# Performance work log

Measured on AMD Instinct MI355X. Metric: run time of the kernel, lower is better.

The kernel has to match this reference:

```python
import jax, jax.numpy as jnp
import numpy as np
import math

N = 10000      # atoms
E = 320000     # neighbor pairs (edges)
NELEM = 3      # species one-hot size
NRAD = 8       # radial channels per component
NB = 8         # bessel basis size
ZETA = 4       # max angular moment
RC = 5.0       # radial cutoff
S = 4          # species embedding size (species_layer_sizes[-1])
NCOMP = (ZETA + 2) * NRAD   # 2-body slice + (ZETA+1) angular slices = 48
FEAT = NCOMP * S            # 192

# multinomial expansion of (r_i . r_j)^l : lxlylz powers and l!/(lx!ly!lz!) norms
_TERMS = []
for l in range(ZETA + 1):
    pw, nm = [], []
    for a in range(l + 1):
        for b in range(l + 1 - a):
            c = l - a - b
            pw.append((a, b, c))
            nm.append(math.factorial(l) / (math.factorial(a) * math.factorial(b) * math.factorial(c)))
    _TERMS.append((np.array(pw, dtype=np.float32), np.array(nm, dtype=np.float32)))


def _silu(x):
    return x * jax.nn.sigmoid(x)


def setup_inputs() -> dict:
    key = jax.random.key(0)
    ks = jax.random.split(key, 12)
    rij = (jax.random.uniform(ks[0], (E, 3), minval=-1.0, maxval=1.0) * (RC / math.sqrt(3.0))).astype(jnp.float32)
    first_atom = jax.random.randint(ks[1], (E,), 0, N, dtype=jnp.int32)
    second_atom = jax.random.randint(ks[2], (E,), 0, N, dtype=jnp.int32)
    species_idx = jax.random.randint(ks[3], (N,), 0, NELEM, dtype=jnp.int32)
    w = lambda k, s: (jax.random.normal(k, s) * 0.1).astype(jnp.float32)
    z = lambda s: jnp.zeros(s, jnp.float32)
    return dict(
        rij=rij, species_idx=species_idx, first_atom=first_atom, second_atom=second_atom,
        Wr1=w(ks[4], (NB, 64)), br1=z((64,)),
        Wr2=w(ks[5], (64, NCOMP)), br2=z((NCOMP,)),
        Ws1=w(ks[6], (NELEM, 16)), bs1=z((16,)),
        Ws2=w(ks[7], (16, S)), bs2=z((S,)),
        Wa1=w(ks[8], (FEAT, 64)), ba1=z((64,)),
        Wa2=w(ks[9], (64, 64)), ba2=z((64,)),
        Wa3=w(ks[10], (64, 1)), ba3=z((1,)),
    )


def reference(rij, species_idx, first_atom, second_atom,
              Wr1, br1, Wr2, br2, Ws1, bs1, Ws2, bs2,
              Wa1, ba1, Wa2, ba2, Wa3, ba3):
    d = jnp.sqrt(jnp.sum(rij * rij, axis=-1) + 1e-12)            # [E]
    rhat = rij / d[:, None]                                       # [E,3]
    fc = jnp.where(d < RC, 0.5 * (jnp.cos(np.pi * d / RC) + 1.0), 0.0)
    n = jnp.arange(1, NB + 1, dtype=rij.dtype)
    bes = jnp.sqrt(2.0 / RC) * jnp.sin(n[None, :] * np.pi * d[:, None] / RC) / d[:, None]  # [E,NB]
    # learned radial functions, all components at once, smoothed by cutoff
    R = _silu(_silu(bes @ Wr1 + br1) @ Wr2 + br2) * fc[:, None]   # [E, NCOMP]
    # species encoder -> per-atom embedding, gathered on neighbor atom j
    onehot = jax.nn.one_hot(species_idx, NELEM, dtype=rij.dtype)  # [N,NELEM]
    semb = jnp.tanh(onehot @ Ws1 + bs1) @ Ws2 + bs2               # [N,S]
    sj = semb[second_atom]                                        # [E,S]
    # 2-body feature
    feats = [jax.ops.segment_sum(R[:, :NRAD, None] * sj[:, None, :], first_atom, num_segments=N)]  # [N,NRAD,S]
    off = NRAD
    for l in range(ZETA + 1):
        pw, nm = _TERMS[l]
        comps = jnp.prod(rhat[:, None, :] ** jnp.asarray(pw)[None, :, :], axis=-1)  # [E,C_l]
        Rl = R[:, off:off + NRAD]
        off += NRAD
        edge = Rl[:, :, None, None] * comps[:, None, :, None] * sj[:, None, None, :]  # [E,NRAD,C_l,S]
        A = jax.ops.segment_sum(edge, first_atom, num_segments=N)                     # [N,NRAD,C_l,S]
        feats.append(jnp.einsum('nrcs,c->nrs', A * A, jnp.asarray(nm)))               # [N,NRAD,S]
    feat = jnp.concatenate(feats, axis=1).reshape(N, -1)          # [N, FEAT]
    h = _silu(feat @ Wa1 + ba1)
    h = _silu(h @ Wa2 + ba2)
    return (h @ Wa3 + ba3)[:, 0]                                  # per-atom energies [N]
```

## Files before the change

kernel.cpp:

```cpp
#include <hip/hip_runtime.h>
#include <math.h>

#define NATOMS 10000
#define NEDGES 320000
#define NBINS  (NATOMS * 4)
#define RC_F 5.0f
#define PI_F 3.14159265358979323846f

#define WS_SEMB   0
#define WS_GTOT   12
#define WS_CNT    16
#define WS_OFFS   40016
#define WS_CURSOR 80016
#define WS_EIDX   120016
#define WS_SA     440096
#define WS_SB     10680096

__device__ __constant__ int   d_PWA[35] = {0, 0,0,1, 0,0,0,1,1,2, 0,0,0,0,1,1,1,2,2,3, 0,0,0,0,0,1,1,1,1,2,2,2,3,3,4};
__device__ __constant__ int   d_PWB[35] = {0, 0,1,0, 0,1,2,0,1,0, 0,1,2,3,0,1,2,0,1,0, 0,1,2,3,4,0,1,2,3,0,1,2,0,1,0};
__device__ __constant__ int   d_PWC[35] = {0, 1,0,0, 2,1,0,1,0,0, 3,2,1,0,2,1,0,1,0,0, 4,3,2,1,0,3,2,1,0,2,1,0,1,0,0};
__device__ __constant__ float d_NM[35]  = {1.f, 1.f,1.f,1.f, 1.f,2.f,1.f,2.f,2.f,1.f,
                                           1.f,3.f,3.f,1.f,3.f,6.f,3.f,3.f,3.f,1.f,
                                           1.f,4.f,6.f,4.f,1.f,4.f,12.f,12.f,4.f,6.f,12.f,6.f,4.f,4.f,1.f};
__device__ __constant__ int   d_LBLK[35]= {0, 1,1,1, 2,2,2,2,2,2, 3,3,3,3,3,3,3,3,3,3, 4,4,4,4,4,4,4,4,4,4,4,4,4,4,4};
__device__ __constant__ int   d_L6[6]   = {0,1,4,10,20,35};

__device__ __forceinline__ float siluf(float x) { return x / (1.0f + __expf(-x)); }

__device__ __forceinline__ float2 f2fma(float2 a, float2 b, float2 c) {
  return make_float2(fmaf(a.x, b.x, c.x), fmaf(a.y, b.y, c.y));
}

__device__ __forceinline__ float psel(float x, int p) {
  float x2 = x * x;
  float r = 1.0f;
  r = (p == 1) ? x : r;
  r = (p == 2) ? x2 : r;
  r = (p == 3) ? x2 * x : r;
  r = (p == 4) ? x2 * x2 : r;
  return r;
}

__global__ void k_init(const float* __restrict__ Ws1, const float* __restrict__ bs1,
                       const float* __restrict__ Ws2, const float* __restrict__ bs2,
                       float* __restrict__ ws)
{
  int tid = blockIdx.x * blockDim.x + threadIdx.x;
  int* cnt = (int*)(ws + WS_CNT);
  if (tid < NBINS) cnt[tid] = 0;
  if (tid == 0) *(int*)(ws + WS_GTOT) = 0;
  if (tid < 12) {
    int t = tid >> 2, s = tid & 3;
    float acc = bs2[s];
    for (int j = 0; j < 16; j++) acc += tanhf(Ws1[t * 16 + j] + bs1[j]) * Ws2[j * 4 + s];
    ws[WS_SEMB + tid] = acc;
  }
}

__global__ void k_hist(const int* __restrict__ first_atom, const int* __restrict__ second_atom,
                       const int* __restrict__ species, float* __restrict__ ws)
{
  int e = blockIdx.x * blockDim.x + threadIdx.x;
  if (e < NEDGES) {
    int* cnt = (int*)(ws + WS_CNT);
    int bin = first_atom[e] * 4 + species[second_atom[e]];
    atomicAdd(&cnt[bin], 1);
  }
}

__global__ __launch_bounds__(256) void k_alloc(float* __restrict__ ws)
{
  const int4* cnt4 = (const int4*)(ws + WS_CNT);
  int4* offs4   = (int4*)(ws + WS_OFFS);
  int4* cursor4 = (int4*)(ws + WS_CURSOR);
  int* gtot = (int*)(ws + WS_GTOT);
  __shared__ int wsum[4];
  __shared__ int sbase;
  int tid = threadIdx.x;
  int lane = tid & 63, wv = tid >> 6;
  int a = blockIdx.x * 256 + tid;
  bool live = (a < NATOMS);
  int4 c = live ? cnt4[a] : make_int4(0, 0, 0, 0);
  int s = c.x + c.y + c.z + c.w;
  int inc = s;
  #pragma unroll
  for (int d = 1; d < 64; d <<= 1) {
    int v = __shfl_up(inc, d, 64);
    if (lane >= d) inc += v;
  }
  if (lane == 63) wsum[wv] = inc;
  __syncthreads();
  if (tid == 0) sbase = atomicAdd(gtot, wsum[0] + wsum[1] + wsum[2] + wsum[3]);
  __syncthreads();
  int woff = sbase;
  for (int w = 0; w < wv; w++) woff += wsum[w];
  int o0 = woff + inc - s;
  if (live) {
    int4 o;
    o.x = o0;
    o.y = o.x + c.x;
    o.z = o.y + c.y;
    o.w = o.z + c.z;
    offs4[a] = o;
    cursor4[a] = o;
  }
}

__global__ __launch_bounds__(256) void k_edge(
    const float* __restrict__ rij, const int* __restrict__ species,
    const int* __restrict__ first_atom, const int* __restrict__ second_atom,
    const float* __restrict__ Wr1, const float* __restrict__ br1,
    const float* __restrict__ Wr2, const float* __restrict__ br2,
    float* __restrict__ ws)
{
  __shared__ __align__(16) float sRec[4][64 * 28];
  int tid = threadIdx.x, lane = tid & 63, wv = tid >> 6;
  int e = blockIdx.x * 256 + tid;
  int* cursor = (int*)(ws + WS_CURSOR);
  int* eidx   = (int*)(ws + WS_EIDX);
  float* myrow = &sRec[wv][lane * 28];

  int a = first_atom[e];
  int t = species[second_atom[e]];
  int pos = atomicAdd(&cursor[a * 4 + t], 1);
  eidx[pos] = e;

  float x = rij[e * 3 + 0], y = rij[e * 3 + 1], z = rij[e * 3 + 2];
  float d = sqrtf(x * x + y * y + z * z + 1e-12f);
  float invd = 1.0f / d;

  float theta = (PI_F / RC_F) * d;
  float s1 = __sinf(theta), c1 = __cosf(theta);
  float fc = (d < RC_F) ? 0.5f * (c1 + 1.0f) : 0.0f;
  float bes[8];
  {
    float sq = sqrtf(2.0f / RC_F) * invd;
    float twoc = 2.0f * c1;
    float sp = 0.0f, sc = s1;
    #pragma unroll
    for (int k = 0; k < 8; k++) {
      bes[k] = sq * sc;
      float sn = twoc * sc - sp;
      sp = sc; sc = sn;
    }
  }

  float h1[64];
  #pragma unroll
  for (int j4 = 0; j4 < 16; j4++) {
    float2 a01 = *(const float2*)&br1[j4 * 4];
    float2 a23 = *(const float2*)&br1[j4 * 4 + 2];
    #pragma unroll
    for (int k = 0; k < 8; k++) {
      float2 b2 = make_float2(bes[k], bes[k]);
      a01 = f2fma(b2, *(const float2*)&Wr1[k * 64 + j4 * 4],     a01);
      a23 = f2fma(b2, *(const float2*)&Wr1[k * 64 + j4 * 4 + 2], a23);
    }
    h1[j4 * 4 + 0] = siluf(a01.x);
    h1[j4 * 4 + 1] = siluf(a01.y);
    h1[j4 * 4 + 2] = siluf(a23.x);
    h1[j4 * 4 + 3] = siluf(a23.y);
  }

  int ebase = blockIdx.x * 256 + wv * 64;
  const float* buf = &sRec[wv][0];
  int f4 = lane & 7;

  for (int j4 = 0; j4 < 6; j4++) {
    float2 a01 = *(const float2*)&br2[j4 * 4];
    float2 a23 = *(const float2*)&br2[j4 * 4 + 2];
    #pragma unroll
    for (int k = 0; k < 64; k++) {
      float2 h2 = make_float2(h1[k], h1[k]);
      a01 = f2fma(h2, *(const float2*)&Wr2[k * 48 + j4 * 4],     a01);
      a23 = f2fma(h2, *(const float2*)&Wr2[k * 48 + j4 * 4 + 2], a23);
    }
    *(float4*)(myrow + j4 * 4) = make_float4(siluf(a01.x) * fc, siluf(a01.y) * fc,
                                             siluf(a23.x) * fc, siluf(a23.y) * fc);
  }
  {
    float* gbase = ws + WS_SA + (size_t)ebase * 32;
    if (f4 < 6) {
      #pragma unroll
      for (int q = 0; q < 8; q++) {
        int g4 = q * 64 + lane;
        float4 v = *(const float4*)(buf + (g4 >> 3) * 28 + f4 * 4);
        *(float4*)(gbase + (size_t)g4 * 4) = v;
      }
    }
  }

  for (int j4 = 6; j4 < 12; j4++) {
    float2 a01 = *(const float2*)&br2[j4 * 4];
    float2 a23 = *(const float2*)&br2[j4 * 4 + 2];
    #pragma unroll
    for (int k = 0; k < 64; k++) {
      float2 h2 = make_float2(h1[k], h1[k]);
      a01 = f2fma(h2, *(const float2*)&Wr2[k * 48 + j4 * 4],     a01);
      a23 = f2fma(h2, *(const float2*)&Wr2[k * 48 + j4 * 4 + 2], a23);
    }
    *(float4*)(myrow + (j4 - 6) * 4) = make_float4(siluf(a01.x) * fc, siluf(a01.y) * fc,
                                                   siluf(a23.x) * fc, siluf(a23.y) * fc);
  }
  *(float4*)(myrow + 24) = make_float4(x * invd, y * invd, z * invd, 0.0f);
  {
    float* gbase = ws + WS_SB + (size_t)ebase * 32;
    if (f4 < 7) {
      #pragma unroll
      for (int q = 0; q < 8; q++) {
        int g4 = q * 64 + lane;
        float4 v = *(const float4*)(buf + (g4 >> 3) * 28 + f4 * 4);
        *(float4*)(gbase + (size_t)g4 * 4) = v;
      }
    }
  }
}

__global__ __launch_bounds__(128) void k_atom(
    const float* __restrict__ ws,
    const float* __restrict__ Wa1, const float* __restrict__ ba1,
    const float* __restrict__ Wa2, const float* __restrict__ ba2,
    const float* __restrict__ Wa3, const float* __restrict__ ba3,
    float* __restrict__ out)
{
  __shared__ __align__(16) float sScr[2][1920];
  int tid = threadIdx.x;
  int lane = tid & 63, wv = tid >> 6;
  int a = blockIdx.x * 2 + wv;
  float* sStage = &sScr[wv][0];
  float* sG     = &sScr[wv][768];
  float* sFeat  = &sScr[wv][1632];
  float* sH     = &sScr[wv][1824];

  const int* eidx = (const int*)(ws + WS_EIDX);
  int4 o = ((const int4*)(ws + WS_OFFS))[a];

  const int c = lane;
  bool isc = (c < 35);
  int pa = 0, pb = 0, pcw = 0, lb = 0;
  if (isc) { pa = d_PWA[c]; pb = d_PWB[c]; pcw = d_PWC[c]; lb = d_LBLK[c]; }
  int rdir = lane - 35;
  bool isd = (rdir >= 0) && (rdir < 8);
  int rl = lane >> 4, fl = lane & 15;
  const float* gsrc = ws + (fl < 6 ? WS_SA : WS_SB);
  int foff = (fl < 6) ? fl : ((fl < 13) ? fl - 6 : 6);

  float2 g2[3][4];
  #pragma unroll
  for (int t2 = 0; t2 < 3; t2++)
    #pragma unroll
    for (int r = 0; r < 4; r++) g2[t2][r] = make_float2(0.f, 0.f);
  float g0[3] = {0.0f, 0.0f, 0.0f};

#define CORE(T) {                                                             \
    const float* rb = buf + j * 64;                                           \
    if (isc) {                                                                \
      float comp = psel(rb[48], pa) * psel(rb[49], pb) * psel(rb[50], pcw);   \
      float2 c2 = make_float2(comp, comp);                                    \
      const float2* r2 = (const float2*)(rb + 8 + 8 * lb);                    \
      g2[T][0] = f2fma(c2, r2[0], g2[T][0]);                                  \
      g2[T][1] = f2fma(c2, r2[1], g2[T][1]);                                  \
      g2[T][2] = f2fma(c2, r2[2], g2[T][2]);                                  \
      g2[T][3] = f2fma(c2, r2[3], g2[T][3]);                                  \
    } else if (isd) {                                                         \
      g0[T] += rb[rdir];                                                      \
    }                                                                         \
  }

#define LOADR(Q, DST) {                                                       \
    int sl_ = (Q) * 4 + rl; if (sl_ >= m) sl_ = m - 1;                        \
    int pk_ = __shfl(packed, sl_, 64);                                        \
    DST = *(const float4*)(gsrc + (size_t)pk_ * 32 + foff * 4);               \
  }

#define RUN(T, LO, HI)                                                        \
  for (int cb = (LO); cb < (HI); cb += 64) {                                  \
    int m = (HI) - cb; if (m > 64) m = 64;                                    \
    int pp = cb + lane;                                                       \
    int packed = eidx[pp < (HI) ? pp : (LO)];                                 \
    int R = (m + 3) >> 2;                                                     \
    float4 v0, v1;                                                            \
    LOADR(0, v0)                                                              \
    if (R > 1) { LOADR(1, v1) } else v1 = v0;                                 \
    int bsel = 0;                                                             \
    for (int r = 0; r < R; r++) {                                             \
      float* buf = sStage + (bsel << 8);                                      \
      bsel = (bsel == 2) ? 0 : bsel + 1;                                      \
      *(float4*)(buf + rl * 64 + fl * 4) = v0;                                \
      v0 = v1;                                                                \
      if (r + 2 < R) LOADR(r + 2, v1)                                         \
      int g = r * 4, gm = m - g; if (gm > 4) gm = 4;                          \
      for (int j = 0; j < gm; j++) CORE(T)                                    \
    }                                                                         \
  }

  RUN(0, o.x, o.y)
  RUN(1, o.y, o.z)
  RUN(2, o.z, o.w)
#undef RUN
#undef CORE
#undef LOADR

  if (isc) {
    #pragma unroll
    for (int t2 = 0; t2 < 3; t2++)
      #pragma unroll
      for (int r = 0; r < 8; r++) {
        float gval = (r & 1) ? g2[t2][r >> 1].y : g2[t2][r >> 1].x;
        sG[(t2 * 8 + r) * 36 + c] = gval;
      }
  } else if (isd) {
    #pragma unroll
    for (int t2 = 0; t2 < 3; t2++) sG[(t2 * 8 + rdir) * 36 + 35] = g0[t2];
  }

  int s = lane & 3;
  float se0 = ws[WS_SEMB + s], se1 = ws[WS_SEMB + 4 + s], se2 = ws[WS_SEMB + 8 + s];
  float fout[3];
  #pragma unroll
  for (int u = 0; u < 3; u++) {
    int f = lane + 64 * u;
    int blk = f >> 5, rr = (f >> 2) & 7;
    float acc;
    if (blk == 0) {
      acc = se0 * sG[(0 + rr) * 36 + 35] + se1 * sG[(8 + rr) * 36 + 35] + se2 * sG[(16 + rr) * 36 + 35];
    } else {
      int c0 = d_L6[blk - 1], c1 = d_L6[blk];
      acc = 0.0f;
      for (int cc = c0; cc < c1; cc++) {
        float A = se0 * sG[(0 + rr) * 36 + cc] + se1 * sG[(8 + rr) * 36 + cc] + se2 * sG[(16 + rr) * 36 + cc];
        acc += d_NM[cc] * A * A;
      }
    }
    fout[u] = acc;
  }
  #pragma unroll
  for (int u = 0; u < 3; u++) sFeat[lane + 64 * u] = fout[u];

  {
    float a0 = 0.f, a1 = 0.f, a2 = 0.f, a3 = 0.f;
    for (int k4 = 0; k4 < 48; k4++) {
      float4 f4 = *(const float4*)(sFeat + k4 * 4);
      const float* w = Wa1 + (k4 * 4) * 64 + lane;
      a0 += f4.x * w[0];
      a1 += f4.y * w[64];
      a2 += f4.z * w[128];
      a3 += f4.w * w[192];
    }
    sH[lane] = siluf(a0 + a1 + a2 + a3 + ba1[lane]);
  }

  {
    float a0 = 0.f, a1 = 0.f, a2 = 0.f, a3 = 0.f;
    for (int k4 = 0; k4 < 16; k4++) {
      float4 h4 = *(const float4*)(sH + k4 * 4);
      const float* w = Wa2 + (k4 * 4) * 64 + lane;
      a0 += h4.x * w[0];
      a1 += h4.y * w[64];
      a2 += h4.z * w[128];
      a3 += h4.w * w[192];
    }
    float h2 = siluf(a0 + a1 + a2 + a3 + ba2[lane]);
    float pr = h2 * Wa3[lane];
    #pragma unroll
    for (int off = 32; off > 0; off >>= 1) pr += __shfl_down(pr, off, 64);
    if (lane == 0) out[a] = pr + ba3[0];
  }
}

extern "C" void kernel_launch(void* const* d_in, const int* in_sizes, int n_in,
                              void* d_out, int out_size, void* d_ws, size_t ws_size,
                              hipStream_t stream)
{
  const float* rij         = (const float*)d_in[0];
  const int*   species     = (const int*)  d_in[1];
  const int*   first_atom  = (const int*)  d_in[2];
  const int*   second_atom = (const int*)  d_in[3];
  const float* Wr1 = (const float*)d_in[4];
  const float* br1 = (const float*)d_in[5];
  const float* Wr2 = (const float*)d_in[6];
  const float* br2 = (const float*)d_in[7];
  const float* Ws1 = (const float*)d_in[8];
  const float* bs1 = (const float*)d_in[9];
  const float* Ws2 = (const float*)d_in[10];
  const float* bs2 = (const float*)d_in[11];
  const float* Wa1 = (const float*)d_in[12];
  const float* ba1 = (const float*)d_in[13];
  const float* Wa2 = (const float*)d_in[14];
  const float* ba2 = (const float*)d_in[15];
  const float* Wa3 = (const float*)d_in[16];
  const float* ba3 = (const float*)d_in[17];
  float* ws  = (float*)d_ws;
  float* out = (float*)d_out;

  k_init<<<(NBINS + 255) / 256, 256, 0, stream>>>(Ws1, bs1, Ws2, bs2, ws);
  k_hist<<<(NEDGES + 255) / 256, 256, 0, stream>>>(first_atom, second_atom, species, ws);
  k_alloc<<<(NATOMS + 255) / 256, 256, 0, stream>>>(ws);
  k_edge<<<NEDGES / 256, 256, 0, stream>>>(rij, species, first_atom, second_atom,
                                           Wr1, br1, Wr2, br2, ws);
  k_atom<<<NATOMS / 2, 128, 0, stream>>>(ws, Wa1, ba1, Wa2, ba2, Wa3, ba3, out);
}
```

Measured before the change: 213.7 us.

## Process four atoms per block and share MLP weight loads across waves

```diff
diff --git a/kernel.cpp b/kernel.cpp
--- a/kernel.cpp
+++ b/kernel.cpp
@@ -216,21 +216,25 @@
   }
 }
 
-__global__ __launch_bounds__(128) void k_atom(
+__global__ __launch_bounds__(256) void k_atom(
     const float* __restrict__ ws,
     const float* __restrict__ Wa1, const float* __restrict__ ba1,
     const float* __restrict__ Wa2, const float* __restrict__ ba2,
     const float* __restrict__ Wa3, const float* __restrict__ ba3,
     float* __restrict__ out)
 {
-  __shared__ __align__(16) float sScr[2][1920];
+  __shared__ __align__(16) float sStage[4][768];
+  __shared__ __align__(16) float sG[4][864];
+  __shared__ __align__(16) float sFeat[4][192];
+  __shared__ __align__(16) float sP[4][4][64];
+  __shared__ __align__(16) float sH[4][64];
+  __shared__ float sSemb[12];
   int tid = threadIdx.x;
   int lane = tid & 63, wv = tid >> 6;
-  int a = blockIdx.x * 2 + wv;
-  float* sStage = &sScr[wv][0];
-  float* sG     = &sScr[wv][768];
-  float* sFeat  = &sScr[wv][1632];
-  float* sH     = &sScr[wv][1824];
+  int a = blockIdx.x * 4 + wv;
+  float* sStg = sStage[wv];
+  float* sGw  = sG[wv];
+  if (tid < 12) sSemb[tid] = ws[WS_SEMB + tid];
 
   const int* eidx = (const int*)(ws + WS_EIDX);
   int4 o = ((const int4*)(ws + WS_OFFS))[a];
@@ -284,7 +288,7 @@
     if (R > 1) { LOADR(1, v1) } else v1 = v0;                                 \
     int bsel = 0;                                                             \
     for (int r = 0; r < R; r++) {                                             \
-      float* buf = sStage + (bsel << 8);                                      \
+      float* buf = sStg + (bsel << 8);                                        \
       bsel = (bsel == 2) ? 0 : bsel + 1;                                      \
       *(float4*)(buf + rl * 64 + fl * 4) = v0;                                \
       v0 = v1;                                                                \
@@ -307,61 +311,95 @@
       #pragma unroll
       for (int r = 0; r < 8; r++) {
         float gval = (r & 1) ? g2[t2][r >> 1].y : g2[t2][r >> 1].x;
-        sG[(t2 * 8 + r) * 36 + c] = gval;
+        sGw[(t2 * 8 + r) * 36 + c] = gval;
       }
   } else if (isd) {
     #pragma unroll
-    for (int t2 = 0; t2 < 3; t2++) sG[(t2 * 8 + rdir) * 36 + 35] = g0[t2];
-  }
-
-  int s = lane & 3;
-  float se0 = ws[WS_SEMB + s], se1 = ws[WS_SEMB + 4 + s], se2 = ws[WS_SEMB + 8 + s];
-  float fout[3];
+    for (int t2 = 0; t2 < 3; t2++) sGw[(t2 * 8 + rdir) * 36 + 35] = g0[t2];
+  }
+  __syncthreads();
+
   #pragma unroll
   for (int u = 0; u < 3; u++) {
-    int f = lane + 64 * u;
-    int blk = f >> 5, rr = (f >> 2) & 7;
+    int idx = tid + 256 * u;
+    int i = idx / 192;
+    int f = idx - i * 192;
+    int s = f & 3, rr = (f >> 2) & 7, blk = f >> 5;
+    float se0 = sSemb[s], se1 = sSemb[4 + s], se2 = sSemb[8 + s];
+    const float* Gi = sG[i];
     float acc;
     if (blk == 0) {
-      acc = se0 * sG[(0 + rr) * 36 + 35] + se1 * sG[(8 + rr) * 36 + 35] + se2 * sG[(16 + rr) * 36 + 35];
+      acc = se0 * Gi[(0 + rr) * 36 + 35] + se1 * Gi[(8 + rr) * 36 + 35] + se2 * Gi[(16 + rr) * 36 + 35];
     } else {
       int c0 = d_L6[blk - 1], c1 = d_L6[blk];
       acc = 0.0f;
       for (int cc = c0; cc < c1; cc++) {
-        float A = se0 * sG[(0 + rr) * 36 + cc] + se1 * sG[(8 + rr) * 36 + cc] + se2 * sG[(16 + rr) * 36 + cc];
+        float A = se0 * Gi[(0 + rr) * 36 + cc] + se1 * Gi[(8 + rr) * 36 + cc] + se2 * Gi[(16 + rr) * 36 + cc];
         acc += d_NM[cc] * A * A;
       }
     }
-    fout[u] = acc;
-  }
-  #pragma unroll
-  for (int u = 0; u < 3; u++) sFeat[lane + 64 * u] = fout[u];
+    sFeat[i][f] = acc;
+  }
+  __syncthreads();
 
   {
     float a0 = 0.f, a1 = 0.f, a2 = 0.f, a3 = 0.f;
-    for (int k4 = 0; k4 < 48; k4++) {
-      float4 f4 = *(const float4*)(sFeat + k4 * 4);
-      const float* w = Wa1 + (k4 * 4) * 64 + lane;
-      a0 += f4.x * w[0];
-      a1 += f4.y * w[64];
-      a2 += f4.z * w[128];
-      a3 += f4.w * w[192];
-    }
-    sH[lane] = siluf(a0 + a1 + a2 + a3 + ba1[lane]);
-  }
+    int k0 = wv * 48;
+    for (int kk = 0; kk < 48; kk += 4) {
+      float4 f0 = *(const float4*)&sFeat[0][k0 + kk];
+      float4 f1 = *(const float4*)&sFeat[1][k0 + kk];
+      float4 f2 = *(const float4*)&sFeat[2][k0 + kk];
+      float4 f3 = *(const float4*)&sFeat[3][k0 + kk];
+      #pragma unroll
+      for (int q = 0; q < 4; q++) {
+        float w = Wa1[(k0 + kk + q) * 64 + lane];
+        float e0 = (q == 0) ? f0.x : (q == 1) ? f0.y : (q == 2) ? f0.z : f0.w;
+        float e1 = (q == 0) ? f1.x : (q == 1) ? f1.y : (q == 2) ? f1.z : f1.w;
+        float e2 = (q == 0) ? f2.x : (q == 1) ? f2.y : (q == 2) ? f2.z : f2.w;
+        float e3 = (q == 0) ? f3.x : (q == 1) ? f3.y : (q == 2) ? f3.z : f3.w;
+        a0 = fmaf(e0, w, a0); a1 = fmaf(e1, w, a1);
+        a2 = fmaf(e2, w, a2); a3 = fmaf(e3, w, a3);
+      }
+    }
+    sP[wv][0][lane] = a0; sP[wv][1][lane] = a1;
+    sP[wv][2][lane] = a2; sP[wv][3][lane] = a3;
+  }
+  __syncthreads();
+  sH[wv][lane] = siluf(sP[0][wv][lane] + sP[1][wv][lane] + sP[2][wv][lane] + sP[3][wv][lane] + ba1[lane]);
+  __syncthreads();
 
   {
     float a0 = 0.f, a1 = 0.f, a2 = 0.f, a3 = 0.f;
-    for (int k4 = 0; k4 < 16; k4++) {
-      float4 h4 = *(const float4*)(sH + k4 * 4);
-      const float* w = Wa2 + (k4 * 4) * 64 + lane;
-      a0 += h4.x * w[0];
-      a1 += h4.y * w[64];
-      a2 += h4.z * w[128];
-      a3 += h4.w * w[192];
-    }
-    float h2 = siluf(a0 + a1 + a2 + a3 + ba2[lane]);
-    float pr = h2 * Wa3[lane];
+    int k0 = wv * 16;
+    for (int kk = 0; kk < 16; kk += 4) {
+      float4 h0 = *(const float4*)&sH[0][k0 + kk];
+      float4 h1v = *(const float4*)&sH[1][k0 + kk];
+      float4 h2v = *(const float4*)&sH[2][k0 + kk];
+      float4 h3 = *(const float4*)&sH[3][k0 + kk];
+      #pragma unroll
+      for (int q = 0; q < 4; q++) {
+        float w = Wa2[(k0 + kk + q) * 64 + lane];
+        float e0 = (q == 0) ? h0.x : (q == 1) ? h0.y : (q == 2) ? h0.z : h0.w;
+        float e1 = (q == 0) ? h1v.x : (q == 1) ? h1v.y : (q == 2) ? h1v.z : h1v.w;
+        float e2 = (q == 0) ? h2v.x : (q == 1) ? h2v.y : (q == 2) ? h2v.z : h2v.w;
+        float e3 = (q == 0) ? h3.x : (q == 1) ? h3.y : (q == 2) ? h3.z : h3.w;
+        a0 = fmaf(e0, w, a0); a1 = fmaf(e1, w, a1);
+        a2 = fmaf(e2, w, a2); a3 = fmaf(e3, w, a3);
+      }
+    }
+    sP[wv][0][lane] = a0; sP[wv][1][lane] = a1;
+    sP[wv][2][lane] = a2; sP[wv][3][lane] = a3;
+  }
+  __syncthreads();
+  {
+    float h2 = siluf(sP[0][wv][lane] + sP[1][wv][lane] + sP[2][wv][lane] + sP[3][wv][lane] + ba2[lane]);
+    float v = h2 * Wa3[lane];
+    __syncthreads();
+    sH[wv][lane] = v;
+  }
+  __syncthreads();
+  {
+    float pr = sH[wv][lane];
     #pragma unroll
     for (int off = 32; off > 0; off >>= 1) pr += __shfl_down(pr, off, 64);
     if (lane == 0) out[a] = pr + ba3[0];
@@ -398,5 +436,5 @@
   k_alloc<<<(NATOMS + 255) / 256, 256, 0, stream>>>(ws);
   k_edge<<<NEDGES / 256, 256, 0, stream>>>(rij, species, first_atom, second_atom,
                                            Wr1, br1, Wr2, br2, ws);
-  k_atom<<<NATOMS / 2, 128, 0, stream>>>(ws, Wa1, ba1, Wa2, ba2, Wa3, ba3, out);
-}
+  k_atom<<<NATOMS / 4, 256, 0, stream>>>(ws, Wa1, ba1, Wa2, ba2, Wa3, ba3, out);
+}
```

New measurement: 220.5 us. 3.2% more time.

## Replace per-edge radial MLP with interpolated lookup table over distance

Applied to the files above, without the earlier changes.

```diff
diff --git a/kernel.cpp b/kernel.cpp
--- a/kernel.cpp
+++ b/kernel.cpp
@@ -6,6 +6,7 @@
 #define NBINS  (NATOMS * 4)
 #define RC_F 5.0f
 #define PI_F 3.14159265358979323846f
+#define TABN 16384
 
 #define WS_SEMB   0
 #define WS_GTOT   12
@@ -15,6 +16,7 @@
 #define WS_EIDX   120016
 #define WS_SA     440096
 #define WS_SB     10680096
+#define WS_TAB    20920096
 
 __device__ __constant__ int   d_PWA[35] = {0, 0,0,1, 0,0,0,1,1,2, 0,0,0,0,1,1,1,2,2,3, 0,0,0,0,0,1,1,1,1,2,2,2,3,3,4};
 __device__ __constant__ int   d_PWB[35] = {0, 0,1,0, 0,1,2,0,1,0, 0,1,2,3,0,1,2,0,1,0, 0,1,2,3,4,0,1,2,3,0,1,2,0,1,0};
@@ -54,6 +56,50 @@
     float acc = bs2[s];
     for (int j = 0; j < 16; j++) acc += tanhf(Ws1[t * 16 + j] + bs1[j]) * Ws2[j * 4 + s];
     ws[WS_SEMB + tid] = acc;
+  }
+}
+
+__global__ __launch_bounds__(256) void k_tab(
+    const float* __restrict__ Wr1, const float* __restrict__ br1,
+    const float* __restrict__ Wr2, const float* __restrict__ br2,
+    float* __restrict__ ws)
+{
+  int i = blockIdx.x * 256 + threadIdx.x;
+  if (i > TABN) return;
+  float d = (float)i * (RC_F / (float)TABN);
+  float theta = (PI_F / RC_F) * d;
+  float s1 = __sinf(theta), c1 = __cosf(theta);
+  float fc = (d < RC_F) ? 0.5f * (c1 + 1.0f) : 0.0f;
+  float bes[8];
+  float sq = sqrtf(2.0f / RC_F);
+  if (i == 0) {
+    #pragma unroll
+    for (int k = 0; k < 8; k++) bes[k] = sq * (float)(k + 1) * (PI_F / RC_F);
+  } else {
+    float invd = 1.0f / d;
+    float twoc = 2.0f * c1;
+    float sp = 0.0f, sc = s1;
+    #pragma unroll
+    for (int k = 0; k < 8; k++) {
+      bes[k] = sq * invd * sc;
+      float sn = twoc * sc - sp;
+      sp = sc; sc = sn;
+    }
+  }
+  float h1[64];
+  #pragma unroll
+  for (int j = 0; j < 64; j++) {
+    float acc = br1[j];
+    #pragma unroll
+    for (int k = 0; k < 8; k++) acc += bes[k] * Wr1[k * 64 + j];
+    h1[j] = siluf(acc);
+  }
+  float* row = ws + WS_TAB + (size_t)i * 48;
+  for (int j = 0; j < 48; j++) {
+    float acc = br2[j];
+    #pragma unroll
+    for (int k = 0; k < 64; k++) acc += h1[k] * Wr2[k * 48 + j];
+    row[j] = siluf(acc) * fc;
   }
 }
 
@@ -109,8 +155,6 @@
 __global__ __launch_bounds__(256) void k_edge(
     const float* __restrict__ rij, const int* __restrict__ species,
     const int* __restrict__ first_atom, const int* __restrict__ second_atom,
-    const float* __restrict__ Wr1, const float* __restrict__ br1,
-    const float* __restrict__ Wr2, const float* __restrict__ br2,
     float* __restrict__ ws)
 {
   __shared__ __align__(16) float sRec[4][64 * 28];
@@ -129,54 +173,24 @@
   float d = sqrtf(x * x + y * y + z * z + 1e-12f);
   float invd = 1.0f / d;
 
-  float theta = (PI_F / RC_F) * d;
-  float s1 = __sinf(theta), c1 = __cosf(theta);
-  float fc = (d < RC_F) ? 0.5f * (c1 + 1.0f) : 0.0f;
-  float bes[8];
-  {
-    float sq = sqrtf(2.0f / RC_F) * invd;
-    float twoc = 2.0f * c1;
-    float sp = 0.0f, sc = s1;
-    #pragma unroll
-    for (int k = 0; k < 8; k++) {
-      bes[k] = sq * sc;
-      float sn = twoc * sc - sp;
-      sp = sc; sc = sn;
-    }
-  }
-
-  float h1[64];
-  #pragma unroll
-  for (int j4 = 0; j4 < 16; j4++) {
-    float2 a01 = *(const float2*)&br1[j4 * 4];
-    float2 a23 = *(const float2*)&br1[j4 * 4 + 2];
-    #pragma unroll
-    for (int k = 0; k < 8; k++) {
-      float2 b2 = make_float2(bes[k], bes[k]);
-      a01 = f2fma(b2, *(const float2*)&Wr1[k * 64 + j4 * 4],     a01);
-      a23 = f2fma(b2, *(const float2*)&Wr1[k * 64 + j4 * 4 + 2], a23);
-    }
-    h1[j4 * 4 + 0] = siluf(a01.x);
-    h1[j4 * 4 + 1] = siluf(a01.y);
-    h1[j4 * 4 + 2] = siluf(a23.x);
-    h1[j4 * 4 + 3] = siluf(a23.y);
-  }
+  float u = d * ((float)TABN / RC_F);
+  int i = (int)u;
+  if (i > TABN - 1) i = TABN - 1;
+  float f = u - (float)i;
+  const float* r0 = ws + WS_TAB + (size_t)i * 48;
+  const float* r1 = r0 + 48;
 
   int ebase = blockIdx.x * 256 + wv * 64;
   const float* buf = &sRec[wv][0];
   int f4 = lane & 7;
 
-  for (int j4 = 0; j4 < 6; j4++) {
-    float2 a01 = *(const float2*)&br2[j4 * 4];
-    float2 a23 = *(const float2*)&br2[j4 * 4 + 2];
-    #pragma unroll
-    for (int k = 0; k < 64; k++) {
-      float2 h2 = make_float2(h1[k], h1[k]);
-      a01 = f2fma(h2, *(const float2*)&Wr2[k * 48 + j4 * 4],     a01);
-      a23 = f2fma(h2, *(const float2*)&Wr2[k * 48 + j4 * 4 + 2], a23);
-    }
-    *(float4*)(myrow + j4 * 4) = make_float4(siluf(a01.x) * fc, siluf(a01.y) * fc,
-                                             siluf(a23.x) * fc, siluf(a23.y) * fc);
+  #pragma unroll
+  for (int q = 0; q < 6; q++) {
+    float4 v0 = *(const float4*)(r0 + q * 4);
+    float4 v1 = *(const float4*)(r1 + q * 4);
+    *(float4*)(myrow + q * 4) = make_float4(
+        fmaf(f, v1.x - v0.x, v0.x), fmaf(f, v1.y - v0.y, v0.y),
+        fmaf(f, v1.z - v0.z, v0.z), fmaf(f, v1.w - v0.w, v0.w));
   }
   {
     float* gbase = ws + WS_SA + (size_t)ebase * 32;
@@ -190,17 +204,13 @@
     }
   }
 
-  for (int j4 = 6; j4 < 12; j4++) {
-    float2 a01 = *(const float2*)&br2[j4 * 4];
-    float2 a23 = *(const float2*)&br2[j4 * 4 + 2];
-    #pragma unroll
-    for (int k = 0; k < 64; k++) {
-      float2 h2 = make_float2(h1[k], h1[k]);
-      a01 = f2fma(h2, *(const float2*)&Wr2[k * 48 + j4 * 4],     a01);
-      a23 = f2fma(h2, *(const float2*)&Wr2[k * 48 + j4 * 4 + 2], a23);
-    }
-    *(float4*)(myrow + (j4 - 6) * 4) = make_float4(siluf(a01.x) * fc, siluf(a01.y) * fc,
-                                                   siluf(a23.x) * fc, siluf(a23.y) * fc);
+  #pragma unroll
+  for (int q = 6; q < 12; q++) {
+    float4 v0 = *(const float4*)(r0 + q * 4);
+    float4 v1 = *(const float4*)(r1 + q * 4);
+    *(float4*)(myrow + (q - 6) * 4) = make_float4(
+        fmaf(f, v1.x - v0.x, v0.x), fmaf(f, v1.y - v0.y, v0.y),
+        fmaf(f, v1.z - v0.z, v0.z), fmaf(f, v1.w - v0.w, v0.w));
   }
   *(float4*)(myrow + 24) = make_float4(x * invd, y * invd, z * invd, 0.0f);
   {
@@ -394,9 +404,9 @@
   float* out = (float*)d_out;
 
   k_init<<<(NBINS + 255) / 256, 256, 0, stream>>>(Ws1, bs1, Ws2, bs2, ws);
+  k_tab<<<(TABN + 256) / 256, 256, 0, stream>>>(Wr1, br1, Wr2, br2, ws);
   k_hist<<<(NEDGES + 255) / 256, 256, 0, stream>>>(first_atom, second_atom, species, ws);
   k_alloc<<<(NATOMS + 255) / 256, 256, 0, stream>>>(ws);
-  k_edge<<<NEDGES / 256, 256, 0, stream>>>(rij, species, first_atom, second_atom,
-                                           Wr1, br1, Wr2, br2, ws);
+  k_edge<<<NEDGES / 256, 256, 0, stream>>>(rij, species, first_atom, second_atom, ws);
   k_atom<<<NATOMS / 2, 128, 0, stream>>>(ws, Wa1, ba1, Wa2, ba2, Wa3, ba3, out);
 }
```

Measured after the change: 225.0 us. 5.3% more time.
